# Kernel optimization log

Measured on AMD Instinct MI355X. Metric: run time of the kernel, lower is better.

Reference implementation:

```python
import jax, jax.numpy as jnp
import numpy as np

B, C, W, H = 16, 512, 32, 32
CQ = C // 2
WSCALE = 0.05  # keep energy logits in a sane range for softmax


def setup_inputs() -> dict:
    key = jax.random.key(0)
    ks = jax.random.split(key, 6)
    return {
        "x": jax.random.normal(ks[0], (B, C, W, H), dtype=jnp.float32),
        "Wq": jax.random.normal(ks[1], (CQ, C), dtype=jnp.float32) * WSCALE,
        "bq": jnp.zeros((CQ,), dtype=jnp.float32),
        "Wk": jax.random.normal(ks[2], (CQ, C), dtype=jnp.float32) * WSCALE,
        "bk": jnp.zeros((CQ,), dtype=jnp.float32),
        "Wv": jax.random.normal(ks[3], (C, C), dtype=jnp.float32) * WSCALE,
        "bv": jnp.zeros((C,), dtype=jnp.float32),
        "Wa": jax.random.normal(ks[4], (1, C), dtype=jnp.float32) * WSCALE,
        "ba": jnp.zeros((1,), dtype=jnp.float32),
        "gamma": jax.random.normal(ks[5], (1,), dtype=jnp.float32) * 0.1,
    }


def reference(x, Wq, bq, Wk, bk, Wv, bv, Wa, ba, gamma):
    b, c, w, h = x.shape
    n = w * h
    xf = x.reshape(b, c, n)  # flatten spatial: B,C,N
    # 1x1 convs == per-position channel matmuls
    q = jnp.einsum('oc,bcn->bon', Wq, xf) + bq[None, :, None]  # B,C/2,N
    k = jnp.einsum('oc,bcn->bon', Wk, xf) + bk[None, :, None]  # B,C/2,N
    v = jnp.einsum('oc,bcn->bon', Wv, xf) + bv[None, :, None]  # B,C,N
    # energy[b,i,j] = <q[:, i], k[:, j]>  (unscaled, single head)
    energy = jnp.einsum('bci,bcj->bij', q, k)  # B,N,N
    attn = jax.nn.softmax(energy, axis=-1)
    # out[b,c,i] = sum_j v[b,c,j] * attn[b,i,j]
    out = jnp.einsum('bcj,bij->bci', v, attn).reshape(b, c, w, h)
    # agnostic gating: 1x1 conv C->1 + sigmoid, gate = 1 - sigmoid
    ag = jax.nn.sigmoid(jnp.einsum('oc,bchw->bohw', Wa, out) + ba[None, :, None, None])
    out_A = out * (1.0 - ag)
    out_final = gamma[0] * out + x
    return (out_final, out_A)
```

## Files before the change

kernel.cpp:

```cpp
#include <hip/hip_runtime.h>
#include <hip/hip_bf16.h>
#include <math.h>

#define B 16
#define C 512
#define CQ 256
#define N 1024

typedef short bf16x8 __attribute__((ext_vector_type(8)));
typedef _Float16 f16x8 __attribute__((ext_vector_type(8)));
typedef float f32x4 __attribute__((ext_vector_type(4)));
typedef unsigned short ushort;

__device__ __forceinline__ unsigned short f2bf(float f) {
    __hip_bfloat16 h = __float2bfloat16(f);
    return *(unsigned short*)&h;
}
__device__ __forceinline__ ushort f2h(float f) {
    _Float16 h = (_Float16)f;
    return *(ushort*)&h;
}
__device__ __forceinline__ float h2f(ushort u) {
    _Float16 h = *(_Float16*)&u;
    return (float)h;
}
__device__ __forceinline__ f16x8 as_h(bf16x8 v) {
    union { bf16x8 s; f16x8 h; } u; u.s = v; return u.h;
}

__device__ __forceinline__ void gload16(void* lds, const void* g) {
    __builtin_amdgcn_global_load_lds(
        (const __attribute__((address_space(1))) void*)g,
        (__attribute__((address_space(3))) void*)lds, 16, 0, 0);
}

__device__ __forceinline__ void barrier_lgkm() {
    asm volatile("s_waitcnt lgkmcnt(0)" ::: "memory");
    __builtin_amdgcn_s_barrier();
    __builtin_amdgcn_sched_barrier(0);
}

__global__ __launch_bounds__(256) void gemm_dual(
    const ushort* __restrict__ xT, const ushort* __restrict__ Wqk,
    const ushort* __restrict__ Wv16,
    ushort* __restrict__ qkT, ushort* __restrict__ v_,
    const float* __restrict__ bqk, const float* __restrict__ bv)
{
    __shared__ __align__(16) ushort As[128 * 128];
    __shared__ __align__(16) ushort Bs[128 * 128];

    const int lin  = blockIdx.x;
    const int half = lin & 1;
    const int slot = lin >> 1;
    const int xcd  = slot & 7;
    const int s2   = slot >> 3;
    const int bz   = xcd + 8 * (s2 >> 5);
    const int wxy  = s2 & 31;
    const int bx   = half ? (wxy & 7) : (wxy & 3);
    const int by   = half ? (wxy >> 3) : (wxy >> 2);

    const ushort* A;  long long sA;
    const ushort* BT; long long sB;
    ushort* Ch;       long long sC;
    const float* bias; int bias_mode; int Ncols;
    if (half == 0) {
        A = xT;   sA = (long long)N * C;  BT = Wqk;  sB = 0;
        Ch = qkT; sC = (long long)N * 512;
        bias = bqk; bias_mode = 2; Ncols = 512;
    } else {
        A = Wv16; sA = 0;                 BT = xT;   sB = (long long)N * C;
        Ch = v_;  sC = (long long)C * N;
        bias = bv;  bias_mode = 1; Ncols = N;
    }
    const int K = C;

    const int tid  = threadIdx.x;
    const int lane = tid & 63;
    const int w    = tid >> 6;
    const int wr   = (w >> 1) * 64;
    const int wc   = (w & 1) * 64;
    const int fr   = lane & 15;
    const int ko2  = (lane >> 4) * 16;

    const int brow = by * 128;
    const int bcol = bx * 128;
    const size_t K2 = (size_t)K * 2;

    const char* Ab = (const char*)(A  + (size_t)bz * sA + (size_t)brow * K);
    const char* Bb = (const char*)(BT + (size_t)bz * sB + (size_t)bcol * K);

    const int sr = tid >> 4;
    const int ss = (tid & 15) * 16;

    f32x4 acc[4][4] = {};

    for (int k0 = 0; k0 < K; k0 += 128) {
#pragma unroll
        for (int p = 0; p < 8; ++p) {
            const int row = p * 16 + sr;
            const size_t so = (size_t)row * K2 + (size_t)k0 * 2
                            + (size_t)(ss ^ ((row & 15) << 4));
            gload16((char*)As + p * 4096 + tid * 16, Ab + so);
            gload16((char*)Bs + p * 4096 + tid * 16, Bb + so);
        }
        __syncthreads();
#pragma unroll
        for (int k32 = 0; k32 < 4; ++k32) {
            const int kswz = (k32 * 64 + ko2) ^ (fr << 4);
            bf16x8 ah[4], bh[4];
#pragma unroll
            for (int m = 0; m < 4; ++m)
                ah[m] = *(const bf16x8*)((const char*)As + (wr + m * 16 + fr) * 256 + kswz);
#pragma unroll
            for (int n = 0; n < 4; ++n)
                bh[n] = *(const bf16x8*)((const char*)Bs + (wc + n * 16 + fr) * 256 + kswz);
#pragma unroll
            for (int m = 0; m < 4; ++m)
#pragma unroll
                for (int n = 0; n < 4; ++n)
                    acc[m][n] = __builtin_amdgcn_mfma_f32_16x16x32_f16(
                        as_h(ah[m]), as_h(bh[n]), acc[m][n], 0, 0, 0);
        }
        __syncthreads();
    }

    const int crow = brow + wr + (lane >> 4) * 4;
    const int ccol = bcol + wc + fr;
    const size_t cbase = (size_t)bz * sC;
#pragma unroll
    for (int m = 0; m < 4; ++m) {
#pragma unroll
        for (int n = 0; n < 4; ++n) {
            const float cb = (bias_mode == 2) ? bias[ccol + n * 16] : 0.f;
#pragma unroll
            for (int r = 0; r < 4; ++r) {
                const int row = crow + m * 16 + r;
                const int col = ccol + n * 16;
                float vv = acc[m][n][r]
                         + ((bias_mode == 1) ? bias[row] : cb);
                Ch[cbase + (size_t)row * Ncols + col] = f2h(vv);
            }
        }
    }
}

__global__ __launch_bounds__(512, 2) void fused_attn(
    const ushort* __restrict__ qk, const ushort* __restrict__ vmat,
    const float* __restrict__ Wa, const float* __restrict__ ba,
    const float* __restrict__ gamma, const float* __restrict__ x,
    float* __restrict__ dout)
{
    __shared__ __align__(16) char lds[149504];
    __shared__ float redbuf[2][2][4][32];
    __shared__ float redA[8][64];
    __shared__ float agL[64];

    const int tid  = threadIdx.x;
    const int lane = tid & 63;
    const int w    = tid >> 6;
    const int g    = w >> 2;
    const int wg4  = w & 3;
    const int fr   = lane & 15;
    const int il0  = (lane >> 4) * 4;
    const int ko2  = (lane >> 4) * 16;

    const int wgid = blockIdx.x + gridDim.x * blockIdx.y;
    const int nid  = (wgid & 7) * 32 + (wgid >> 3);
    const int b    = nid >> 4;
    const int i0   = (nid & 15) * 64;

    const char* qkB = (const char*)qk + (size_t)b * N * 1024;
    const char* vB  = (const char*)vmat + (size_t)b * C * N * 2;

    const int srow = tid >> 4;
    const int ssg  = (tid & 15) * 16;

    f16x8 a_h[2][2][4];
#pragma unroll
    for (int ks0 = 0; ks0 < 2; ++ks0)
#pragma unroll
        for (int m = 0; m < 2; ++m) {
            const char* qr = qkB + (size_t)(i0 + g * 32 + m * 16 + fr) * 1024
                           + ks0 * 256 + (lane >> 4) * 16;
#pragma unroll
            for (int k32 = 0; k32 < 4; ++k32)
                a_h[ks0][m][k32] = *(const f16x8*)(qr + k32 * 64);
        }

    auto stageK = [&](int s) {
        const int jt_  = s & 7;
        const int ks0_ = s >> 3;
        char* dst = lds + (s & 3) * 32768;
#pragma unroll
        for (int p = 0; p < 4; ++p) {
            const int row = p * 32 + srow;
            const size_t so = (size_t)(jt_ * 128 + row) * 1024 + 512
                            + (size_t)(ks0_ * 256)
                            + (size_t)(ssg ^ ((row & 15) << 4));
            gload16(dst + p * 8192 + tid * 16, qkB + so);
        }
    };

    f32x4 acc[16][2];
#pragma unroll
    for (int jt = 0; jt < 16; ++jt)
#pragma unroll
        for (int m = 0; m < 2; ++m)
            acc[jt][m] = (f32x4){0.f, 0.f, 0.f, 0.f};

    stageK(0);
    stageK(1);

#pragma unroll
    for (int s = 0; s < 16; ++s) {
        if (s + 2 < 16) stageK(s + 2);
        if (s < 14)       asm volatile("s_waitcnt vmcnt(8)" ::: "memory");
        else if (s == 14) asm volatile("s_waitcnt vmcnt(4)" ::: "memory");
        else              asm volatile("s_waitcnt vmcnt(0)" ::: "memory");
        __builtin_amdgcn_s_barrier();
        __builtin_amdgcn_sched_barrier(0);
        const char* kb = lds + (s & 3) * 32768;
        const int ks0 = s >> 3;
        __builtin_amdgcn_s_setprio(1);
#pragma unroll
        for (int sub = 0; sub < 2; ++sub) {
            const int jrow = sub * 64 + wg4 * 16 + fr;
            const int rb   = jrow * 256;
            const int jidx = (s & 7) * 2 + sub;
#pragma unroll
            for (int k32 = 0; k32 < 4; ++k32) {
                const int kswz = (k32 * 64 + ko2) ^ (fr << 4);
                f16x8 b_h = *(const f16x8*)(kb + rb + kswz);
#pragma unroll
                for (int m = 0; m < 2; ++m)
                    acc[jidx][m] = __builtin_amdgcn_mfma_f32_16x16x32_f16(
                        a_h[ks0][m][k32], b_h, acc[jidx][m], 0, 0, 0);
            }
        }
        __builtin_amdgcn_s_setprio(0);
    }

    auto stageV = [&](int j) {
        char* dst = lds + (j & 1) * 65536;
#pragma unroll
        for (int p = 0; p < 8; ++p) {
            const int ch = p * 512 + tid;
            const int row = ch >> 3;
            const int sg  = (ch & 7) * 16;
            const size_t so = (size_t)row * (N * 2) + (size_t)(j * 128)
                            + (size_t)(sg ^ ((row & 7) << 4));
            gload16(dst + ch * 16, vB + so);
        }
    };
    stageV(0);

    float mx[2][4];
#pragma unroll
    for (int m = 0; m < 2; ++m)
#pragma unroll
        for (int r = 0; r < 4; ++r) {
            float v = acc[0][m][r];
#pragma unroll
            for (int jt = 1; jt < 16; ++jt) v = fmaxf(v, acc[jt][m][r]);
            mx[m][r] = v;
        }
#pragma unroll
    for (int off = 1; off < 16; off <<= 1)
#pragma unroll
        for (int m = 0; m < 2; ++m)
#pragma unroll
            for (int r = 0; r < 4; ++r)
                mx[m][r] = fmaxf(mx[m][r], __shfl_xor(mx[m][r], off, 64));
    if (fr == 0) {
#pragma unroll
        for (int m = 0; m < 2; ++m)
#pragma unroll
            for (int r = 0; r < 4; ++r)
                redbuf[0][g][wg4][m * 16 + il0 + r] = mx[m][r];
    }
    barrier_lgkm();
#pragma unroll
    for (int m = 0; m < 2; ++m)
#pragma unroll
        for (int r = 0; r < 4; ++r) {
            const int row = m * 16 + il0 + r;
            mx[m][r] = fmaxf(fmaxf(redbuf[0][g][0][row], redbuf[0][g][1][row]),
                             fmaxf(redbuf[0][g][2][row], redbuf[0][g][3][row]));
        }

    float sm[2][4] = {};
#pragma unroll
    for (int jt = 0; jt < 16; ++jt)
#pragma unroll
        for (int m = 0; m < 2; ++m) {
            f32x4 e;
#pragma unroll
            for (int r = 0; r < 4; ++r) {
                e[r] = __expf(acc[jt][m][r] - mx[m][r]);
                sm[m][r] += e[r];
            }
            acc[jt][m] = e;
        }
#pragma unroll
    for (int off = 1; off < 16; off <<= 1)
#pragma unroll
        for (int m = 0; m < 2; ++m)
#pragma unroll
            for (int r = 0; r < 4; ++r)
                sm[m][r] += __shfl_xor(sm[m][r], off, 64);
    if (fr == 0) {
#pragma unroll
        for (int m = 0; m < 2; ++m)
#pragma unroll
            for (int r = 0; r < 4; ++r)
                redbuf[1][g][wg4][m * 16 + il0 + r] = sm[m][r];
    }
    barrier_lgkm();
#pragma unroll
    for (int m = 0; m < 2; ++m)
#pragma unroll
        for (int r = 0; r < 4; ++r) {
            const int row = m * 16 + il0 + r;
            float s = redbuf[1][g][0][row] + redbuf[1][g][1][row]
                    + redbuf[1][g][2][row] + redbuf[1][g][3][row];
            mx[m][r] = 1.f / s;
        }

    char* pPb = lds + 131072;
    f32x4 apv[4][4] = {};

#pragma unroll
    for (int jt = 0; jt < 16; ++jt) {
        ushort* pS = (ushort*)(pPb + (jt & 1) * 9216);
#pragma unroll
        for (int m = 0; m < 2; ++m) {
            const int lr = g * 32 + m * 16 + il0;
#pragma unroll
            for (int r = 0; r < 4; ++r)
                pS[(lr + r) * 72 + wg4 * 16 + fr] = f2h(acc[jt][m][r] * mx[m][r]);
        }
        asm volatile("s_waitcnt vmcnt(0) lgkmcnt(0)" ::: "memory");
        __builtin_amdgcn_s_barrier();
        __builtin_amdgcn_sched_barrier(0);
        if (jt + 1 < 16) stageV(jt + 1);
        const char* vb = lds + (jt & 1) * 65536;
#pragma unroll
        for (int k32 = 0; k32 < 2; ++k32) {
            f16x8 af[4], bf[4];
#pragma unroll
            for (int cf = 0; cf < 4; ++cf) {
                const int row = w * 64 + cf * 16 + fr;
                const int kb  = (k32 * 64 + ko2) ^ ((fr & 7) << 4);
                af[cf] = *(const f16x8*)(vb + row * 128 + kb);
            }
#pragma unroll
            for (int f = 0; f < 4; ++f)
                bf[f] = *(const f16x8*)((const char*)pS
                        + (f * 16 + fr) * 144 + k32 * 64 + ko2);
            __builtin_amdgcn_s_setprio(1);
#pragma unroll
            for (int cf = 0; cf < 4; ++cf)
#pragma unroll
                for (int f = 0; f < 4; ++f)
                    apv[cf][f] = __builtin_amdgcn_mfma_f32_16x16x32_f16(
                        af[cf], bf[f], apv[cf][f], 0, 0, 0);
            __builtin_amdgcn_s_setprio(0);
        }
    }

    float pg[4] = {0.f, 0.f, 0.f, 0.f};
#pragma unroll
    for (int cf = 0; cf < 4; ++cf)
#pragma unroll
        for (int r = 0; r < 4; ++r) {
            const float wv = Wa[w * 64 + cf * 16 + il0 + r];
#pragma unroll
            for (int f = 0; f < 4; ++f)
                pg[f] += wv * apv[cf][f][r];
        }
#pragma unroll
    for (int off = 16; off < 64; off <<= 1)
#pragma unroll
        for (int f = 0; f < 4; ++f)
            pg[f] += __shfl_xor(pg[f], off, 64);
    if (lane < 16) {
#pragma unroll
        for (int f = 0; f < 4; ++f)
            redA[w][f * 16 + fr] = pg[f];
    }
    barrier_lgkm();
    if (tid < 64) {
        float s = ba[0];
#pragma unroll
        for (int k = 0; k < 8; ++k) s += redA[k][tid];
        agL[tid] = 1.f / (1.f + __expf(-s));
    }

    const size_t BCN = (size_t)B * C * N;
    const float gmm = gamma[0];
    float* oS = (float*)lds;

#pragma unroll
    for (int h = 0; h < 2; ++h) {
        f32x4 xv[8];
#pragma unroll
        for (int p = 0; p < 8; ++p) {
            const int ch  = p * 512 + tid;
            const int row = ch >> 3;
            const int sg  = ch & 7;
            const int ib  = h * 32 + sg * 4;
            const size_t idx = ((size_t)b * C + row) * N + i0 + ib;
            xv[p] = *(const f32x4*)&x[idx];
        }
#pragma unroll
        for (int cf = 0; cf < 4; ++cf) {
            const int crow = w * 64 + cf * 16 + il0;
#pragma unroll
            for (int f = 0; f < 2; ++f) {
                const int col = f * 16 + fr;
#pragma unroll
                for (int r = 0; r < 4; ++r)
                    oS[(crow + r) * 33 + col] = apv[cf][2 * h + f][r];
            }
        }
        barrier_lgkm();
#pragma unroll
        for (int p = 0; p < 8; ++p) {
            const int ch  = p * 512 + tid;
            const int row = ch >> 3;
            const int sg  = ch & 7;
            const int ib  = h * 32 + sg * 4;
            f32x4 o = *(const f32x4*)&oS[row * 33 + sg * 4];
            const size_t idx = ((size_t)b * C + row) * N + i0 + ib;
            f32x4 of, oa;
#pragma unroll
            for (int q = 0; q < 4; ++q) {
                of[q] = gmm * o[q] + xv[p][q];
                oa[q] = o[q] * (1.f - agL[ib + q]);
            }
            *(f32x4*)&dout[idx]       = of;
            *(f32x4*)&dout[BCN + idx] = oa;
        }
        barrier_lgkm();
    }
}

__global__ void transpose_x_f16(const float* __restrict__ x,
                                ushort* __restrict__ xT) {
    __shared__ float t[32][33];
    int b  = blockIdx.z;
    int c0 = blockIdx.y * 32;
    int n0 = blockIdx.x * 32;
    int tid = threadIdx.x;
    int tx = tid & 31;
    int ty = tid >> 5;
#pragma unroll
    for (int r = 0; r < 4; ++r)
        t[ty + r * 8][tx] = x[(size_t)b * C * N + (size_t)(c0 + ty + r * 8) * N + n0 + tx];
    __syncthreads();
#pragma unroll
    for (int r = 0; r < 4; ++r) {
        float v = t[tx][ty + r * 8];
        size_t idx = (size_t)b * N * C + (size_t)(n0 + ty + r * 8) * C + c0 + tx;
        xT[idx] = f2h(v);
    }
}

__global__ void prep_weights(const float* __restrict__ Wq, const float* __restrict__ Wk,
                             const float* __restrict__ Wv,
                             const float* __restrict__ bq, const float* __restrict__ bk,
                             ushort* __restrict__ Wqk, ushort* __restrict__ Wv16,
                             float* __restrict__ bqk) {
    int i = blockIdx.x * 256 + threadIdx.x;
    if (i < CQ * C) {
        Wqk[i]          = f2h(Wq[i]);
        Wqk[CQ * C + i] = f2h(Wk[i]);
    }
    if (i < C * C) Wv16[i] = f2h(Wv[i]);
    if (i < 512) bqk[i] = (i < CQ) ? bq[i] : bk[i - CQ];
}

extern "C" void kernel_launch(void* const* d_in, const int* in_sizes, int n_in,
                              void* d_out, int out_size, void* d_ws, size_t ws_size,
                              hipStream_t stream) {
    const float* x     = (const float*)d_in[0];
    const float* Wq    = (const float*)d_in[1];
    const float* bq    = (const float*)d_in[2];
    const float* Wk    = (const float*)d_in[3];
    const float* bk    = (const float*)d_in[4];
    const float* Wv    = (const float*)d_in[5];
    const float* bv    = (const float*)d_in[6];
    const float* Wa    = (const float*)d_in[7];
    const float* ba    = (const float*)d_in[8];
    const float* gamma = (const float*)d_in[9];
    float* out = (float*)d_out;

    const size_t MB = 1048576;
    char* ws = (char*)d_ws;
    ushort* v_     = (ushort*)(ws);
    ushort* qkT    = (ushort*)(ws + 16 * MB);
    ushort* Wqk    = (ushort*)(ws + 48 * MB);
    ushort* Wv16   = (ushort*)(ws + 48 * MB + 524288);
    float*  bqk    = (float*)(ws + 49 * MB);
    ushort* xT     = (ushort*)(ws + 80 * MB);
    const size_t need = 96 * MB;
    if (ws_size < need) return;

    dim3 blk(256);
    transpose_x_f16<<<dim3(N / 32, C / 32, B), blk, 0, stream>>>(x, xT);
    prep_weights<<<dim3(C * C / 256), blk, 0, stream>>>(
        Wq, Wk, Wv, bq, bk, Wqk, Wv16, bqk);

    gemm_dual<<<dim3(1024), blk, 0, stream>>>(
        xT, Wqk, Wv16, qkT, v_, bqk, bv);

    fused_attn<<<dim3(16, 16), dim3(512), 0, stream>>>(
        qkT, v_, Wa, ba, gamma, x, out);
}
```

Baseline: 114.1 us.

## Deepen PV pipeline, fuse weight prep into transpose, remap GEMM blocks

The PV stage of the attention kernel now uses 32 smaller steps with a 4-deep V staging ring and a P repack that is interleaved ahead of each step. This replaces the 16-step double-buffered loop that waited on all outstanding loads every iteration. Weight conversion is folded into the transpose kernel, which removes one launch. GEMM block indices are remapped so each XCD gets a different interleaving of the two GEMM halves. The setprio hints are removed and the x loads in the epilogue are moved next to their use, which lowers register pressure but may expose load latency.

```diff
diff --git a/kernel.cpp b/kernel.cpp
--- a/kernel.cpp
+++ b/kernel.cpp
@@ -11,18 +11,11 @@
 typedef _Float16 f16x8 __attribute__((ext_vector_type(8)));
 typedef float f32x4 __attribute__((ext_vector_type(4)));
 typedef unsigned short ushort;
-
-__device__ __forceinline__ unsigned short f2bf(float f) {
-    __hip_bfloat16 h = __float2bfloat16(f);
-    return *(unsigned short*)&h;
-}
+typedef ushort u16x4 __attribute__((ext_vector_type(4)));
+
 __device__ __forceinline__ ushort f2h(float f) {
     _Float16 h = (_Float16)f;
     return *(ushort*)&h;
-}
-__device__ __forceinline__ float h2f(ushort u) {
-    _Float16 h = *(_Float16*)&u;
-    return (float)h;
 }
 __device__ __forceinline__ f16x8 as_h(bf16x8 v) {
     union { bf16x8 s; f16x8 h; } u; u.s = v; return u.h;
@@ -40,7 +33,7 @@
     __builtin_amdgcn_sched_barrier(0);
 }
 
-__global__ __launch_bounds__(256) void gemm_dual(
+__global__ __launch_bounds__(256) void gemm_merged(
     const ushort* __restrict__ xT, const ushort* __restrict__ Wqk,
     const ushort* __restrict__ Wv16,
     ushort* __restrict__ qkT, ushort* __restrict__ v_,
@@ -50,24 +43,24 @@
     __shared__ __align__(16) ushort Bs[128 * 128];
 
     const int lin  = blockIdx.x;
-    const int half = lin & 1;
-    const int slot = lin >> 1;
-    const int xcd  = slot & 7;
-    const int s2   = slot >> 3;
-    const int bz   = xcd + 8 * (s2 >> 5);
-    const int wxy  = s2 & 31;
-    const int bx   = half ? (wxy & 7) : (wxy & 3);
-    const int by   = half ? (wxy >> 3) : (wxy >> 2);
-
+    const int xcd  = lin & 7;
+    const int half = (lin >> 3) & 1;
+    const int slot = lin >> 4;
+    const int bz   = xcd + 8 * (slot >> 5);
+    const int wxy  = slot & 31;
+
+    int bx, by;
     const ushort* A;  long long sA;
     const ushort* BT; long long sB;
     ushort* Ch;       long long sC;
     const float* bias; int bias_mode; int Ncols;
     if (half == 0) {
+        bx = wxy & 3; by = wxy >> 2;
         A = xT;   sA = (long long)N * C;  BT = Wqk;  sB = 0;
         Ch = qkT; sC = (long long)N * 512;
         bias = bqk; bias_mode = 2; Ncols = 512;
     } else {
+        bx = wxy & 7; by = wxy >> 3;
         A = Wv16; sA = 0;                 BT = xT;   sB = (long long)N * C;
         Ch = v_;  sC = (long long)C * N;
         bias = bv;  bias_mode = 1; Ncols = N;
@@ -136,8 +129,7 @@
             for (int r = 0; r < 4; ++r) {
                 const int row = crow + m * 16 + r;
                 const int col = ccol + n * 16;
-                float vv = acc[m][n][r]
-                         + ((bias_mode == 1) ? bias[row] : cb);
+                float vv = acc[m][n][r] + ((bias_mode == 1) ? bias[row] : cb);
                 Ch[cbase + (size_t)row * Ncols + col] = f2h(vv);
             }
         }
@@ -221,7 +213,6 @@
         __builtin_amdgcn_sched_barrier(0);
         const char* kb = lds + (s & 3) * 32768;
         const int ks0 = s >> 3;
-        __builtin_amdgcn_s_setprio(1);
 #pragma unroll
         for (int sub = 0; sub < 2; ++sub) {
             const int jrow = sub * 64 + wg4 * 16 + fr;
@@ -237,22 +228,22 @@
                         a_h[ks0][m][k32], b_h, acc[jidx][m], 0, 0, 0);
             }
         }
-        __builtin_amdgcn_s_setprio(0);
-    }
-
-    auto stageV = [&](int j) {
-        char* dst = lds + (j & 1) * 65536;
-#pragma unroll
-        for (int p = 0; p < 8; ++p) {
-            const int ch = p * 512 + tid;
-            const int row = ch >> 3;
-            const int sg  = (ch & 7) * 16;
-            const size_t so = (size_t)row * (N * 2) + (size_t)(j * 128)
-                            + (size_t)(sg ^ ((row & 7) << 4));
+    }
+
+    auto stageV32 = [&](int s) {
+        char* dst = lds + (s & 3) * 32768;
+#pragma unroll
+        for (int p = 0; p < 4; ++p) {
+            const int ch  = p * 512 + tid;
+            const int row = ch >> 2;
+            const int sg  = (ch & 3) * 16;
+            const size_t so = (size_t)row * (N * 2) + (size_t)(s * 64)
+                            + (size_t)(sg ^ ((row & 3) << 4));
             gload16(dst + ch * 16, vB + so);
         }
     };
-    stageV(0);
+    stageV32(0);
+    stageV32(1);
 
     float mx[2][4];
 #pragma unroll
@@ -329,43 +320,51 @@
     char* pPb = lds + 131072;
     f32x4 apv[4][4] = {};
 
-#pragma unroll
-    for (int jt = 0; jt < 16; ++jt) {
-        ushort* pS = (ushort*)(pPb + (jt & 1) * 9216);
-#pragma unroll
-        for (int m = 0; m < 2; ++m) {
-            const int lr = g * 32 + m * 16 + il0;
-#pragma unroll
-            for (int r = 0; r < 4; ++r)
-                pS[(lr + r) * 72 + wg4 * 16 + fr] = f2h(acc[jt][m][r] * mx[m][r]);
-        }
-        asm volatile("s_waitcnt vmcnt(0) lgkmcnt(0)" ::: "memory");
+    auto repackP = [&](int s) {
+        if ((wg4 >> 1) == (s & 1)) {
+            ushort* pS = (ushort*)(pPb + (s & 3) * 4608);
+            const int jidx = s >> 1;
+            const int colj = (wg4 & 1) * 16 + fr;
+#pragma unroll
+            for (int m = 0; m < 2; ++m) {
+                const int lr = g * 32 + m * 16 + il0;
+#pragma unroll
+                for (int r = 0; r < 4; ++r)
+                    pS[(lr + r) * 36 + colj] = f2h(acc[jidx][m][r] * mx[m][r]);
+            }
+        }
+    };
+    repackP(0);
+    repackP(1);
+
+#pragma unroll
+    for (int s = 0; s < 32; ++s) {
+        if (s + 2 < 32) {
+            stageV32(s + 2);
+            repackP(s + 2);
+        }
+        if (s < 30)       asm volatile("s_waitcnt vmcnt(8) lgkmcnt(0)" ::: "memory");
+        else if (s == 30) asm volatile("s_waitcnt vmcnt(4) lgkmcnt(0)" ::: "memory");
+        else              asm volatile("s_waitcnt vmcnt(0) lgkmcnt(0)" ::: "memory");
         __builtin_amdgcn_s_barrier();
         __builtin_amdgcn_sched_barrier(0);
-        if (jt + 1 < 16) stageV(jt + 1);
-        const char* vb = lds + (jt & 1) * 65536;
-#pragma unroll
-        for (int k32 = 0; k32 < 2; ++k32) {
-            f16x8 af[4], bf[4];
-#pragma unroll
-            for (int cf = 0; cf < 4; ++cf) {
-                const int row = w * 64 + cf * 16 + fr;
-                const int kb  = (k32 * 64 + ko2) ^ ((fr & 7) << 4);
-                af[cf] = *(const f16x8*)(vb + row * 128 + kb);
-            }
+        const char* vb = lds + (s & 3) * 32768;
+        const char* pS = pPb + (s & 3) * 4608;
+        f16x8 af[4], bf[4];
+#pragma unroll
+        for (int cf = 0; cf < 4; ++cf) {
+            const int row = w * 64 + cf * 16 + fr;
+            af[cf] = *(const f16x8*)(vb + row * 64 + (ko2 ^ ((row & 3) << 4)));
+        }
+#pragma unroll
+        for (int f = 0; f < 4; ++f)
+            bf[f] = *(const f16x8*)(pS + (f * 16 + fr) * 72 + ko2);
+#pragma unroll
+        for (int cf = 0; cf < 4; ++cf)
 #pragma unroll
             for (int f = 0; f < 4; ++f)
-                bf[f] = *(const f16x8*)((const char*)pS
-                        + (f * 16 + fr) * 144 + k32 * 64 + ko2);
-            __builtin_amdgcn_s_setprio(1);
-#pragma unroll
-            for (int cf = 0; cf < 4; ++cf)
-#pragma unroll
-                for (int f = 0; f < 4; ++f)
-                    apv[cf][f] = __builtin_amdgcn_mfma_f32_16x16x32_f16(
-                        af[cf], bf[f], apv[cf][f], 0, 0, 0);
-            __builtin_amdgcn_s_setprio(0);
-        }
+                apv[cf][f] = __builtin_amdgcn_mfma_f32_16x16x32_f16(
+                    af[cf], bf[f], apv[cf][f], 0, 0, 0);
     }
 
     float pg[4] = {0.f, 0.f, 0.f, 0.f};
@@ -402,16 +401,6 @@
 
 #pragma unroll
     for (int h = 0; h < 2; ++h) {
-        f32x4 xv[8];
-#pragma unroll
-        for (int p = 0; p < 8; ++p) {
-            const int ch  = p * 512 + tid;
-            const int row = ch >> 3;
-            const int sg  = ch & 7;
-            const int ib  = h * 32 + sg * 4;
-            const size_t idx = ((size_t)b * C + row) * N + i0 + ib;
-            xv[p] = *(const f32x4*)&x[idx];
-        }
 #pragma unroll
         for (int cf = 0; cf < 4; ++cf) {
             const int crow = w * 64 + cf * 16 + il0;
@@ -432,10 +421,11 @@
             const int ib  = h * 32 + sg * 4;
             f32x4 o = *(const f32x4*)&oS[row * 33 + sg * 4];
             const size_t idx = ((size_t)b * C + row) * N + i0 + ib;
+            f32x4 xv = *(const f32x4*)&x[idx];
             f32x4 of, oa;
 #pragma unroll
             for (int q = 0; q < 4; ++q) {
-                of[q] = gmm * o[q] + xv[p][q];
+                of[q] = gmm * o[q] + xv[q];
                 oa[q] = o[q] * (1.f - agL[ib + q]);
             }
             *(f32x4*)&dout[idx]       = of;
@@ -445,13 +435,33 @@
     }
 }
 
-__global__ void transpose_x_f16(const float* __restrict__ x,
-                                ushort* __restrict__ xT) {
+__global__ void transpose_prep(const float* __restrict__ x,
+                               ushort* __restrict__ xT,
+                               const float* __restrict__ Wq,
+                               const float* __restrict__ Wk,
+                               const float* __restrict__ Wv,
+                               const float* __restrict__ bq,
+                               const float* __restrict__ bk,
+                               ushort* __restrict__ Wqk,
+                               ushort* __restrict__ Wv16,
+                               float* __restrict__ bqk) {
     __shared__ float t[32][33];
+    int tid = threadIdx.x;
+
+    const int linwg = blockIdx.x + 32 * (blockIdx.y + 16 * blockIdx.z);
+    if (linwg < 1024) {
+        int i = linwg * 256 + tid;
+        if (i < CQ * C) {
+            Wqk[i]          = f2h(Wq[i]);
+            Wqk[CQ * C + i] = f2h(Wk[i]);
+        }
+        if (i < C * C) Wv16[i] = f2h(Wv[i]);
+        if (i < 512) bqk[i] = (i < CQ) ? bq[i] : bk[i - CQ];
+    }
+
     int b  = blockIdx.z;
     int c0 = blockIdx.y * 32;
     int n0 = blockIdx.x * 32;
-    int tid = threadIdx.x;
     int tx = tid & 31;
     int ty = tid >> 5;
 #pragma unroll
@@ -464,20 +474,6 @@
         size_t idx = (size_t)b * N * C + (size_t)(n0 + ty + r * 8) * C + c0 + tx;
         xT[idx] = f2h(v);
     }
-}
-
-__global__ void prep_weights(const float* __restrict__ Wq, const float* __restrict__ Wk,
-                             const float* __restrict__ Wv,
-                             const float* __restrict__ bq, const float* __restrict__ bk,
-                             ushort* __restrict__ Wqk, ushort* __restrict__ Wv16,
-                             float* __restrict__ bqk) {
-    int i = blockIdx.x * 256 + threadIdx.x;
-    if (i < CQ * C) {
-        Wqk[i]          = f2h(Wq[i]);
-        Wqk[CQ * C + i] = f2h(Wk[i]);
-    }
-    if (i < C * C) Wv16[i] = f2h(Wv[i]);
-    if (i < 512) bqk[i] = (i < CQ) ? bq[i] : bk[i - CQ];
 }
 
 extern "C" void kernel_launch(void* const* d_in, const int* in_sizes, int n_in,
@@ -507,11 +503,10 @@
     if (ws_size < need) return;
 
     dim3 blk(256);
-    transpose_x_f16<<<dim3(N / 32, C / 32, B), blk, 0, stream>>>(x, xT);
-    prep_weights<<<dim3(C * C / 256), blk, 0, stream>>>(
-        Wq, Wk, Wv, bq, bk, Wqk, Wv16, bqk);
-
-    gemm_dual<<<dim3(1024), blk, 0, stream>>>(
+    transpose_prep<<<dim3(N / 32, C / 32, B), blk, 0, stream>>>(
+        x, xT, Wq, Wk, Wv, bq, bk, Wqk, Wv16, bqk);
+
+    gemm_merged<<<dim3(1024), blk, 0, stream>>>(
         xT, Wqk, Wv16, qkT, v_, bqk, bv);
 
     fused_attn<<<dim3(16, 16), dim3(512), 0, stream>>>(
```

Measured after the change: 128.6 us. +12.7%, slower.
